# Performance work log

Measured on AMD Instinct MI355X. Metric: run time of the kernel, lower is better.

The kernel has to match this reference:

```python
import jax, jax.numpy as jnp
import numpy as np

TEMPERATURE = 0.07
EPS = 1e-12  # F.normalize eps


def _l2_normalize(x):
    # matches torch F.normalize(dim=1): x / max(||x||, eps)
    n = jnp.linalg.norm(x, axis=1, keepdims=True)
    return x / jnp.maximum(n, EPS)


def setup_inputs() -> dict:
    key = jax.random.key(0)
    k1, k2 = jax.random.split(key)
    N, Z = 4096, 256
    z1 = jax.random.normal(k1, (N, Z), dtype=jnp.float32)
    z2 = jax.random.normal(k2, (N, Z), dtype=jnp.float32)
    return {"z1": z1, "z2": z2}


def reference(z1, z2):
    N = z1.shape[0]
    z1n = _l2_normalize(z1)
    z2n = _l2_normalize(z2)
    reps = jnp.concatenate([z1n, z2n], axis=0)          # [2N, Z]
    sim = reps @ reps.T                                  # cosine sim (rows unit-norm)
    # positives: sim[i, i+N] for i<N and sim[i, i-N] for i>=N
    pos = jnp.concatenate([jnp.diagonal(sim, offset=N),
                           jnp.diagonal(sim, offset=-N)])  # [2N]
    # The row logits are {positive} U {all sims except self and positive},
    # i.e. all entries except the self-similarity diagonal.
    inv_t = 1.0 / TEMPERATURE
    twoN = 2 * N
    diag_mask = jnp.eye(twoN, dtype=bool)
    logits = jnp.where(diag_mask, -jnp.inf, sim * inv_t)   # [2N, 2N]
    lse = jax.nn.logsumexp(logits, axis=1)                 # [2N]
    # cross_entropy with label at the positive: -pos/T + lse, sum / 2N
    loss = jnp.mean(lse - pos * inv_t)
    return loss
```

## Files before the change

kernel.cpp:

```cpp
#include <hip/hip_runtime.h>
#include <hip/hip_bf16.h>

#define N_ROWS 4096
#define TWO_N  8192
#define ZDIM   256
#define INV_T  (1.0f/0.07f)
#define EXP_SCALE (INV_T * 1.44269504088896340736f)

typedef __attribute__((ext_vector_type(4))) float f32x4;

__device__ __forceinline__ void async_load16(const void* g, void* lds_uniform_base) {
  __builtin_amdgcn_global_load_lds(
      (const __attribute__((address_space(1))) void*)g,
      (__attribute__((address_space(3))) void*)lds_uniform_base, 16, 0, 0);
}

__device__ __forceinline__ unsigned char f32_to_e4m3(float x) {
  unsigned int u = __float_as_uint(x);
  const unsigned int s = u >> 31;
  unsigned int a = u & 0x7FFFFFFFu;
  if (a > 0x43E00000u) a = 0x43E00000u;
  const float f = __uint_as_float(a);
  unsigned int out;
  if (a < (121u << 23)) {
    const int m = (int)rintf(f * 512.0f);
    out = (unsigned int)m;
  } else {
    const unsigned int r = a + 0x7FFFFu + ((a >> 20) & 1u);
    const unsigned int e8 = (r >> 23) - 120u;
    out = (e8 << 3) | ((r >> 20) & 7u);
  }
  return (unsigned char)(out | (s << 7));
}

__global__ __launch_bounds__(256) void normalize_kernel(
    const float* __restrict__ z1, const float* __restrict__ z2,
    unsigned char* __restrict__ reps, float* __restrict__ pos,
    float* __restrict__ out) {
  const int b = blockIdx.x;
  const int t = threadIdx.x;
  const float x1 = z1[b * ZDIM + t];
  const float x2 = z2[b * ZDIM + t];
  float s1 = x1 * x1, s2 = x2 * x2, s3 = x1 * x2;
  #pragma unroll
  for (int m = 1; m < 64; m <<= 1) {
    s1 += __shfl_xor(s1, m, 64);
    s2 += __shfl_xor(s2, m, 64);
    s3 += __shfl_xor(s3, m, 64);
  }
  __shared__ float red[3][4];
  const int w = t >> 6, l = t & 63;
  if (l == 0) { red[0][w] = s1; red[1][w] = s2; red[2][w] = s3; }
  __syncthreads();
  const float n1 = red[0][0] + red[0][1] + red[0][2] + red[0][3];
  const float n2 = red[1][0] + red[1][1] + red[1][2] + red[1][3];
  const float dt = red[2][0] + red[2][1] + red[2][2] + red[2][3];
  const float inv1 = 1.0f / fmaxf(sqrtf(n1), 1e-12f);
  const float inv2 = 1.0f / fmaxf(sqrtf(n2), 1e-12f);
  reps[b * ZDIM + t]            = f32_to_e4m3(x1 * inv1);
  reps[(b + N_ROWS) * ZDIM + t] = f32_to_e4m3(x2 * inv2);
  if (t == 0) {
    pos[b] = dt * inv1 * inv2;
    if (b == 0) out[0] = INV_T;
  }
}

__global__ __launch_bounds__(256, 2) void simsum_kernel(
    const unsigned char* __restrict__ reps,
    float* __restrict__ rowscratch,
    float* __restrict__ colscratch) {
  __shared__ __align__(16) unsigned char Alds[128 * 256];
  __shared__ __align__(16) unsigned char Blds[128 * 256];
  __shared__ float colred[2][256];

  const int tid  = threadIdx.x;
  const int lane = tid & 63;
  const int wave = tid >> 6;
  const int wm = wave >> 1, wn = wave & 1;
  const int quad = lane >> 4;
  const int l16  = lane & 15;
  const int itile = blockIdx.x;
  const int chunk = blockIdx.y;
  const int rowBase = itile * 128;
  const char* gbase = (const char*)reps;

  #pragma unroll
  for (int p = 0; p < 8; ++p) {
    const int c = p * 256 + (wave << 6) + lane;
    const int row = c >> 4, k16 = c & 15;
    const int src = (k16 & 8) | ((k16 ^ row) & 7);
    async_load16(gbase + (rowBase + row) * ZDIM + src * 16,
                 (char*)Alds + (size_t)c * 16 - (size_t)lane * 16 + (size_t)lane * 16);
  }
  __syncthreads();

  const int nd = (chunk == 0) ? ((itile < 32) ? 5 : 4) : 4;

  float rowpart[16];
  #pragma unroll
  for (int i = 0; i < 16; ++i) rowpart[i] = 0.0f;

  const f32x4 zero4 = {0.0f, 0.0f, 0.0f, 0.0f};

  for (int td = 0; td < nd; ++td) {
    const int d = (chunk == 0) ? ((td == 4) ? 32 : td) : (chunk * 4 + td);
    const int jtile = (itile + d) & 63;
    const int colBase = jtile * 128;
    const bool diag = (d == 0);

    if (!diag) {
      __syncthreads();
      #pragma unroll
      for (int p = 0; p < 8; ++p) {
        const int c = p * 256 + (wave << 6) + lane;
        const int row = c >> 4, k16 = c & 15;
        const int src = (k16 & 8) | ((k16 ^ row) & 7);
        async_load16(gbase + (colBase + row) * ZDIM + src * 16, (char*)Blds + c * 16);
      }
      __syncthreads();
    }

    f32x4 acc[4][4];
    #pragma unroll
    for (int mi = 0; mi < 4; ++mi)
      #pragma unroll
      for (int ni = 0; ni < 4; ++ni) acc[mi][ni] = zero4;

    #pragma unroll
    for (int kc = 0; kc < 4; ++kc) {
      #pragma unroll
      for (int kk2 = 0; kk2 < 2; ++kk2) {
        const int CH = kc * 8 + kk2 * 4 + quad;
        const int k16 = CH >> 1, half = (CH & 1) * 8;
        long afrag[4], bfrag[4];
        #pragma unroll
        for (int mi = 0; mi < 4; ++mi) {
          const int m = wm * 64 + mi * 16 + l16;
          const int sw = (k16 & 8) | ((k16 ^ m) & 7);
          afrag[mi] = *(const long*)((const char*)Alds + m * 256 + sw * 16 + half);
        }
        #pragma unroll
        for (int ni = 0; ni < 4; ++ni) {
          const int n = wn * 64 + ni * 16 + l16;
          const int sw = (k16 & 8) | ((k16 ^ n) & 7);
          const char* src = diag ? (const char*)Alds : (const char*)Blds;
          bfrag[ni] = *(const long*)(src + n * 256 + sw * 16 + half);
        }
        #pragma unroll
        for (int mi = 0; mi < 4; ++mi)
          #pragma unroll
          for (int ni = 0; ni < 4; ++ni)
            acc[mi][ni] = __builtin_amdgcn_mfma_f32_16x16x32_fp8_fp8(
                afrag[mi], bfrag[ni], acc[mi][ni], 0, 0, 0);
      }
    }

    float colpart[4] = {0.0f, 0.0f, 0.0f, 0.0f};
    #pragma unroll
    for (int mi = 0; mi < 4; ++mi) {
      #pragma unroll
      for (int r = 0; r < 4; ++r) {
        const int grow = rowBase + wm * 64 + mi * 16 + quad * 4 + r;
        float s = 0.0f;
        #pragma unroll
        for (int ni = 0; ni < 4; ++ni) {
          const int gcol = colBase + wn * 64 + ni * 16 + l16;
          const float v = acc[mi][ni][r];
          const float e = exp2f((v - 1.0f) * EXP_SCALE);
          if (!diag || grow != gcol) s += e;
          colpart[ni] += e;
        }
        rowpart[mi * 4 + r] += s;
      }
    }
    if (!diag) {
      #pragma unroll
      for (int ni = 0; ni < 4; ++ni) {
        float v = colpart[ni];
        v += __shfl_xor(v, 16, 64);
        v += __shfl_xor(v, 32, 64);
        if (quad == 0) colred[td & 1][wm * 128 + wn * 64 + ni * 16 + l16] = v;
      }
      __syncthreads();
      if (tid < 128)
        colscratch[(jtile * 32 + (d - 1)) * 128 + tid] =
            colred[td & 1][tid] + colred[td & 1][128 + tid];
    }
  }

  #pragma unroll
  for (int i = 0; i < 16; ++i) {
    float v = rowpart[i];
    v += __shfl_xor(v, 1, 64);
    v += __shfl_xor(v, 2, 64);
    v += __shfl_xor(v, 4, 64);
    v += __shfl_xor(v, 8, 64);
    rowpart[i] = v;
  }
  __syncthreads();
  if (l16 == 0) {
    #pragma unroll
    for (int mi = 0; mi < 4; ++mi)
      #pragma unroll
      for (int r = 0; r < 4; ++r)
        colred[0][wn * 128 + wm * 64 + mi * 16 + quad * 4 + r] = rowpart[mi * 4 + r];
  }
  __syncthreads();
  if (tid < 128)
    rowscratch[(itile * 8 + chunk) * 128 + tid] = colred[0][tid] + colred[0][128 + tid];
}

__global__ __launch_bounds__(256) void reduce_kernel(
    const float* __restrict__ rowscratch, const float* __restrict__ colscratch,
    const float* __restrict__ pos, float* __restrict__ out) {
  const int j = blockIdx.x;
  const int tid = threadIdx.x;
  float v = 0.0f;
  if (tid < 128) {
    float s = 0.0f;
    #pragma unroll
    for (int c = 0; c < 8; ++c) s += rowscratch[(j * 8 + c) * 128 + tid];
    const int ns = (j < 32) ? 31 : 32;
    for (int si = 0; si < ns; ++si) s += colscratch[(j * 32 + si) * 128 + tid];
    v = logf(s) * (1.0f / (float)TWO_N);
  } else if (tid < 192) {
    v = -pos[j * 64 + (tid - 128)] * (INV_T / (float)N_ROWS);
  }
  #pragma unroll
  for (int m = 1; m < 64; m <<= 1) v += __shfl_xor(v, m, 64);
  __shared__ float red[4];
  if ((tid & 63) == 0) red[tid >> 6] = v;
  __syncthreads();
  if (tid == 0) atomicAdd(out, red[0] + red[1] + red[2] + red[3]);
}

extern "C" void kernel_launch(void* const* d_in, const int* in_sizes, int n_in,
                              void* d_out, int out_size, void* d_ws, size_t ws_size,
                              hipStream_t stream) {
  const float* z1 = (const float*)d_in[0];
  const float* z2 = (const float*)d_in[1];
  char* ws = (char*)d_ws;
  unsigned char* reps = (unsigned char*)ws;
  size_t off = (size_t)TWO_N * ZDIM;
  float* pos = (float*)(ws + off);        off += N_ROWS * 4;
  float* rowscratch = (float*)(ws + off); off += 64 * 8 * 128 * 4;
  float* colscratch = (float*)(ws + off); off += 64 * 32 * 128 * 4;

  normalize_kernel<<<N_ROWS, 256, 0, stream>>>(z1, z2, reps, pos, (float*)d_out);
  simsum_kernel<<<dim3(64, 8), 256, 0, stream>>>(reps, rowscratch, colscratch);
  reduce_kernel<<<64, 256, 0, stream>>>(rowscratch, colscratch, pos, (float*)d_out);
}
```

Measured before the change: 100.5 us.

## Double-buffer B tiles by K-halves and vectorize normalize to one wave per row

The similarity kernel now splits each B column tile into two K-halves held in a double-buffered LDS array and prefetches the next half while MFMAs run on the current one. This replaces the load-then-sync-then-compute pattern and hides global-to-LDS latency. The diagonal tile gets its own path, and the A-tile load addressing is simplified. The normalize kernel is reworked to one wave per row with float4 loads and uchar4 stores, which removes the LDS reduction and block sync. The cost is an extra barrier per half-tile and more complex indexing and swizzle logic.

```diff
diff --git a/kernel.cpp b/kernel.cpp
--- a/kernel.cpp
+++ b/kernel.cpp
@@ -37,31 +37,32 @@
     const float* __restrict__ z1, const float* __restrict__ z2,
     unsigned char* __restrict__ reps, float* __restrict__ pos,
     float* __restrict__ out) {
-  const int b = blockIdx.x;
-  const int t = threadIdx.x;
-  const float x1 = z1[b * ZDIM + t];
-  const float x2 = z2[b * ZDIM + t];
-  float s1 = x1 * x1, s2 = x2 * x2, s3 = x1 * x2;
+  const int lane = threadIdx.x & 63;
+  const int wave = threadIdx.x >> 6;
+  const int r = blockIdx.x * 4 + wave;
+  const float4 a = ((const float4*)(z1 + (size_t)r * ZDIM))[lane];
+  const float4 b = ((const float4*)(z2 + (size_t)r * ZDIM))[lane];
+  float s1 = a.x*a.x + a.y*a.y + a.z*a.z + a.w*a.w;
+  float s2 = b.x*b.x + b.y*b.y + b.z*b.z + b.w*b.w;
+  float s3 = a.x*b.x + a.y*b.y + a.z*b.z + a.w*b.w;
   #pragma unroll
   for (int m = 1; m < 64; m <<= 1) {
     s1 += __shfl_xor(s1, m, 64);
     s2 += __shfl_xor(s2, m, 64);
     s3 += __shfl_xor(s3, m, 64);
   }
-  __shared__ float red[3][4];
-  const int w = t >> 6, l = t & 63;
-  if (l == 0) { red[0][w] = s1; red[1][w] = s2; red[2][w] = s3; }
-  __syncthreads();
-  const float n1 = red[0][0] + red[0][1] + red[0][2] + red[0][3];
-  const float n2 = red[1][0] + red[1][1] + red[1][2] + red[1][3];
-  const float dt = red[2][0] + red[2][1] + red[2][2] + red[2][3];
-  const float inv1 = 1.0f / fmaxf(sqrtf(n1), 1e-12f);
-  const float inv2 = 1.0f / fmaxf(sqrtf(n2), 1e-12f);
-  reps[b * ZDIM + t]            = f32_to_e4m3(x1 * inv1);
-  reps[(b + N_ROWS) * ZDIM + t] = f32_to_e4m3(x2 * inv2);
-  if (t == 0) {
-    pos[b] = dt * inv1 * inv2;
-    if (b == 0) out[0] = INV_T;
+  const float inv1 = 1.0f / fmaxf(sqrtf(s1), 1e-12f);
+  const float inv2 = 1.0f / fmaxf(sqrtf(s2), 1e-12f);
+  uchar4 pa, pb;
+  pa.x = f32_to_e4m3(a.x * inv1); pa.y = f32_to_e4m3(a.y * inv1);
+  pa.z = f32_to_e4m3(a.z * inv1); pa.w = f32_to_e4m3(a.w * inv1);
+  pb.x = f32_to_e4m3(b.x * inv2); pb.y = f32_to_e4m3(b.y * inv2);
+  pb.z = f32_to_e4m3(b.z * inv2); pb.w = f32_to_e4m3(b.w * inv2);
+  ((uchar4*)(reps + (size_t)r * ZDIM))[lane] = pa;
+  ((uchar4*)(reps + (size_t)(r + N_ROWS) * ZDIM))[lane] = pb;
+  if (lane == 0) {
+    pos[r] = s3 * inv1 * inv2;
+    if (r == 0) out[0] = INV_T;
   }
 }
 
@@ -70,7 +71,7 @@
     float* __restrict__ rowscratch,
     float* __restrict__ colscratch) {
   __shared__ __align__(16) unsigned char Alds[128 * 256];
-  __shared__ __align__(16) unsigned char Blds[128 * 256];
+  __shared__ __align__(16) unsigned char Blds[2][128 * 128];
   __shared__ float colred[2][256];
 
   const int tid  = threadIdx.x;
@@ -83,108 +84,168 @@
   const int chunk = blockIdx.y;
   const int rowBase = itile * 128;
   const char* gbase = (const char*)reps;
-
-  #pragma unroll
-  for (int p = 0; p < 8; ++p) {
-    const int c = p * 256 + (wave << 6) + lane;
-    const int row = c >> 4, k16 = c & 15;
-    const int src = (k16 & 8) | ((k16 ^ row) & 7);
-    async_load16(gbase + (rowBase + row) * ZDIM + src * 16,
-                 (char*)Alds + (size_t)c * 16 - (size_t)lane * 16 + (size_t)lane * 16);
-  }
-  __syncthreads();
-
-  const int nd = (chunk == 0) ? ((itile < 32) ? 5 : 4) : 4;
+  const bool diaghere = (chunk == 0);
+
+  {
+    const int r0 = tid >> 4;
+    const int src = (tid & 8) | ((tid ^ (tid >> 4)) & 7);
+    const char* g0 = gbase + (rowBase + r0) * ZDIM + src * 16;
+    char* l0 = (char*)Alds + (wave << 10);
+    #pragma unroll
+    for (int p = 0; p < 8; ++p)
+      async_load16(g0 + p * 16 * ZDIM, l0 + p * 4096);
+  }
+
+  int doff[4];
+  int noff;
+  if (diaghere) {
+    doff[0] = 1; doff[1] = 2; doff[2] = 3; doff[3] = 32;
+    noff = (itile < 32) ? 4 : 3;
+  } else {
+    doff[0] = chunk * 4; doff[1] = chunk * 4 + 1;
+    doff[2] = chunk * 4 + 2; doff[3] = chunk * 4 + 3;
+    noff = 4;
+  }
+  const int Q = noff * 2;
+
+#define STAGE_B(q_) do {                                                        \
+    const int t_ = (q_) >> 1, c_ = (q_) & 1;                                    \
+    const int jt_ = (itile + doff[t_]) & 63;                                    \
+    const int r0_ = tid >> 3;                                        \
+    const int src_ = (tid ^ (tid >> 3)) & 7;                                    \
+    const char* g0_ = gbase + (jt_ * 128 + r0_) * ZDIM + c_ * 128 + src_ * 16;  \
+    char* l0_ = (char*)Blds[c_] + (wave << 10);                                 \
+    _Pragma("unroll")                                                           \
+    for (int p_ = 0; p_ < 4; ++p_)                                              \
+      async_load16(g0_ + p_ * 32 * ZDIM, l0_ + p_ * 4096);                      \
+  } while (0)
 
   float rowpart[16];
   #pragma unroll
   for (int i = 0; i < 16; ++i) rowpart[i] = 0.0f;
-
   const f32x4 zero4 = {0.0f, 0.0f, 0.0f, 0.0f};
 
-  for (int td = 0; td < nd; ++td) {
-    const int d = (chunk == 0) ? ((td == 4) ? 32 : td) : (chunk * 4 + td);
-    const int jtile = (itile + d) & 63;
-    const int colBase = jtile * 128;
-    const bool diag = (d == 0);
-
-    if (!diag) {
-      __syncthreads();
-      #pragma unroll
-      for (int p = 0; p < 8; ++p) {
-        const int c = p * 256 + (wave << 6) + lane;
-        const int row = c >> 4, k16 = c & 15;
-        const int src = (k16 & 8) | ((k16 ^ row) & 7);
-        async_load16(gbase + (colBase + row) * ZDIM + src * 16, (char*)Blds + c * 16);
-      }
-      __syncthreads();
+  if (diaghere) {
+    __syncthreads();
+    if (Q > 0) STAGE_B(0);
+    f32x4 acc[4][4];
+    #pragma unroll
+    for (int mi = 0; mi < 4; ++mi)
+      #pragma unroll
+      for (int ni = 0; ni < 4; ++ni) acc[mi][ni] = zero4;
+    #pragma unroll
+    for (int w = 0; w < 8; ++w) {
+      const int o = w * 4 + quad;
+      const int k16 = o >> 1, half = (o & 1) * 8;
+      long afrag[4], bfrag[4];
+      #pragma unroll
+      for (int mi = 0; mi < 4; ++mi) {
+        const int m = wm * 64 + mi * 16 + l16;
+        const int sw = (k16 & 8) | ((k16 ^ m) & 7);
+        afrag[mi] = *(const long*)((const char*)Alds + m * 256 + sw * 16 + half);
+      }
+      #pragma unroll
+      for (int ni = 0; ni < 4; ++ni) {
+        const int n = wn * 64 + ni * 16 + l16;
+        const int sw = (k16 & 8) | ((k16 ^ n) & 7);
+        bfrag[ni] = *(const long*)((const char*)Alds + n * 256 + sw * 16 + half);
+      }
+      #pragma unroll
+      for (int mi = 0; mi < 4; ++mi)
+        #pragma unroll
+        for (int ni = 0; ni < 4; ++ni)
+          acc[mi][ni] = __builtin_amdgcn_mfma_f32_16x16x32_fp8_fp8(
+              afrag[mi], bfrag[ni], acc[mi][ni], 0, 0, 0);
     }
-
-    f32x4 acc[4][4];
     #pragma unroll
     for (int mi = 0; mi < 4; ++mi)
-      #pragma unroll
-      for (int ni = 0; ni < 4; ++ni) acc[mi][ni] = zero4;
-
-    #pragma unroll
-    for (int kc = 0; kc < 4; ++kc) {
-      #pragma unroll
-      for (int kk2 = 0; kk2 < 2; ++kk2) {
-        const int CH = kc * 8 + kk2 * 4 + quad;
-        const int k16 = CH >> 1, half = (CH & 1) * 8;
-        long afrag[4], bfrag[4];
-        #pragma unroll
-        for (int mi = 0; mi < 4; ++mi) {
-          const int m = wm * 64 + mi * 16 + l16;
-          const int sw = (k16 & 8) | ((k16 ^ m) & 7);
-          afrag[mi] = *(const long*)((const char*)Alds + m * 256 + sw * 16 + half);
-        }
-        #pragma unroll
-        for (int ni = 0; ni < 4; ++ni) {
-          const int n = wn * 64 + ni * 16 + l16;
-          const int sw = (k16 & 8) | ((k16 ^ n) & 7);
-          const char* src = diag ? (const char*)Alds : (const char*)Blds;
-          bfrag[ni] = *(const long*)(src + n * 256 + sw * 16 + half);
-        }
-        #pragma unroll
-        for (int mi = 0; mi < 4; ++mi)
-          #pragma unroll
-          for (int ni = 0; ni < 4; ++ni)
-            acc[mi][ni] = __builtin_amdgcn_mfma_f32_16x16x32_fp8_fp8(
-                afrag[mi], bfrag[ni], acc[mi][ni], 0, 0, 0);
-      }
-    }
-
-    float colpart[4] = {0.0f, 0.0f, 0.0f, 0.0f};
-    #pragma unroll
-    for (int mi = 0; mi < 4; ++mi) {
       #pragma unroll
       for (int r = 0; r < 4; ++r) {
         const int grow = rowBase + wm * 64 + mi * 16 + quad * 4 + r;
         float s = 0.0f;
         #pragma unroll
         for (int ni = 0; ni < 4; ++ni) {
-          const int gcol = colBase + wn * 64 + ni * 16 + l16;
-          const float v = acc[mi][ni][r];
-          const float e = exp2f((v - 1.0f) * EXP_SCALE);
-          if (!diag || grow != gcol) s += e;
-          colpart[ni] += e;
+          const int gcol = rowBase + wn * 64 + ni * 16 + l16;
+          const float e = exp2f((acc[mi][ni][r] - 1.0f) * EXP_SCALE);
+          if (grow != gcol) s += e;
         }
         rowpart[mi * 4 + r] += s;
       }
+    __syncthreads();
+  } else {
+    STAGE_B(0);
+    __syncthreads();
+  }
+
+  f32x4 acc[4][4];
+  for (int q = 0; q < Q; ++q) {
+    if (q + 1 < Q) STAGE_B(q + 1);
+    const int t = q >> 1, c = q & 1;
+    const int d = doff[t];
+    const int jtile = (itile + d) & 63;
+    const int colBase = jtile * 128;
+
+    if (c == 0) {
+      #pragma unroll
+      for (int mi = 0; mi < 4; ++mi)
+        #pragma unroll
+        for (int ni = 0; ni < 4; ++ni) acc[mi][ni] = zero4;
     }
-    if (!diag) {
+    #pragma unroll
+    for (int ws = 0; ws < 4; ++ws) {
+      const int o  = c * 16 + ws * 4 + quad;
+      const int k16 = o >> 1, half = (o & 1) * 8;
+      const int ol = ws * 4 + quad;
+      const int k16l = ol >> 1, halfl = (ol & 1) * 8;
+      long afrag[4], bfrag[4];
+      #pragma unroll
+      for (int mi = 0; mi < 4; ++mi) {
+        const int m = wm * 64 + mi * 16 + l16;
+        const int sw = (k16 & 8) | ((k16 ^ m) & 7);
+        afrag[mi] = *(const long*)((const char*)Alds + m * 256 + sw * 16 + half);
+      }
+      #pragma unroll
+      for (int ni = 0; ni < 4; ++ni) {
+        const int n = wn * 64 + ni * 16 + l16;
+        const int sw = (k16l ^ n) & 7;
+        bfrag[ni] = *(const long*)((const char*)Blds[c] + n * 128 + sw * 16 + halfl);
+      }
+      #pragma unroll
+      for (int mi = 0; mi < 4; ++mi)
+        #pragma unroll
+        for (int ni = 0; ni < 4; ++ni)
+          acc[mi][ni] = __builtin_amdgcn_mfma_f32_16x16x32_fp8_fp8(
+              afrag[mi], bfrag[ni], acc[mi][ni], 0, 0, 0);
+    }
+
+    if (c == 1) {
+      float colpart[4] = {0.0f, 0.0f, 0.0f, 0.0f};
+      #pragma unroll
+      for (int mi = 0; mi < 4; ++mi)
+        #pragma unroll
+        for (int r = 0; r < 4; ++r) {
+          float s = 0.0f;
+          #pragma unroll
+          for (int ni = 0; ni < 4; ++ni) {
+            const float e = exp2f((acc[mi][ni][r] - 1.0f) * EXP_SCALE);
+            s += e;
+            colpart[ni] += e;
+          }
+          rowpart[mi * 4 + r] += s;
+        }
       #pragma unroll
       for (int ni = 0; ni < 4; ++ni) {
         float v = colpart[ni];
         v += __shfl_xor(v, 16, 64);
         v += __shfl_xor(v, 32, 64);
-        if (quad == 0) colred[td & 1][wm * 128 + wn * 64 + ni * 16 + l16] = v;
+        if (quad == 0) colred[t & 1][wm * 128 + wn * 64 + ni * 16 + l16] = v;
       }
       __syncthreads();
       if (tid < 128)
         colscratch[(jtile * 32 + (d - 1)) * 128 + tid] =
-            colred[td & 1][tid] + colred[td & 1][128 + tid];
+            colred[t & 1][tid] + colred[t & 1][128 + tid];
+    } else {
+      __syncthreads();
     }
   }
 
@@ -208,6 +269,7 @@
   __syncthreads();
   if (tid < 128)
     rowscratch[(itile * 8 + chunk) * 128 + tid] = colred[0][tid] + colred[0][128 + tid];
+#undef STAGE_B
 }
 
 __global__ __launch_bounds__(256) void reduce_kernel(
@@ -246,7 +308,7 @@
   float* rowscratch = (float*)(ws + off); off += 64 * 8 * 128 * 4;
   float* colscratch = (float*)(ws + off); off += 64 * 32 * 128 * 4;
 
-  normalize_kernel<<<N_ROWS, 256, 0, stream>>>(z1, z2, reps, pos, (float*)d_out);
+  normalize_kernel<<<1024, 256, 0, stream>>>(z1, z2, reps, pos, (float*)d_out);
   simsum_kernel<<<dim3(64, 8), 256, 0, stream>>>(reps, rowscratch, colscratch);
   reduce_kernel<<<64, 256, 0, stream>>>(rowscratch, colscratch, pos, (float*)d_out);
 }
```

Result: faster. 95.85 us (-4.7%).
